# Optimization experiments

Hardware: AMD Instinct MI355X
Metric: run time of the kernel (lower is better)

The kernel has to match this reference:

```python
import jax, jax.numpy as jnp
import numpy as np

B, D, H, T = 8192, 256, 266, 20  # batch, dim, dim+10, num timesteps
LAMBDA = 1.0
SIGMA = 1.0
EPS = 1e-5  # torch BatchNorm1d default eps


def _bn(h, g, b):
    # training-mode BatchNorm1d: biased batch statistics over axis 0
    m = h.mean(0)
    v = h.var(0)
    return g * (h - m) * jax.lax.rsqrt(v + EPS) + b


def _hidden(x, W, b, g, be):
    return jax.nn.relu(_bn(x @ W.T + b, g, be))


def setup_inputs() -> dict:
    key = jax.random.key(0)
    ks = jax.random.split(key, 16)

    def n(k, shape, s=0.05):
        return jax.random.normal(k, shape, jnp.float32) * s

    inp = {}
    inp["x"] = jax.random.normal(ks[0], (B, D), jnp.float32)
    inp["xi"] = jax.random.normal(ks[1], (T, B, D), jnp.float32)
    inp["timegrid"] = jnp.linspace(0.0, 1.0, T + 1).astype(jnp.float32)
    # per-timestep stacks of Linear+BN params (i_h1, h1_h2, h2_o)
    inp["W1"] = n(ks[2], (T, H, D)); inp["b1"] = jnp.zeros((T, H), jnp.float32)
    inp["g1"] = jnp.ones((T, H), jnp.float32); inp["be1"] = jnp.zeros((T, H), jnp.float32)
    inp["W2"] = n(ks[3], (T, H, H)); inp["b2"] = jnp.zeros((T, H), jnp.float32)
    inp["g2"] = jnp.ones((T, H), jnp.float32); inp["be2"] = jnp.zeros((T, H), jnp.float32)
    inp["W3"] = n(ks[4], (T, D, H)); inp["b3"] = jnp.zeros((T, D), jnp.float32)
    # v0 network: hiddenLayer(D,H) -> hiddenLayer(H,H) -> hiddenLayer(H,1)
    inp["vW1"] = n(ks[5], (H, D)); inp["vb1"] = jnp.zeros((H,), jnp.float32)
    inp["vg1"] = jnp.ones((H,), jnp.float32); inp["vbe1"] = jnp.zeros((H,), jnp.float32)
    inp["vW2"] = n(ks[6], (H, H)); inp["vb2"] = jnp.zeros((H,), jnp.float32)
    inp["vg2"] = jnp.ones((H,), jnp.float32); inp["vbe2"] = jnp.zeros((H,), jnp.float32)
    inp["vW3"] = n(ks[7], (1, H)); inp["vb3"] = jnp.zeros((1,), jnp.float32)
    inp["vg3"] = jnp.ones((1,), jnp.float32); inp["vbe3"] = jnp.zeros((1,), jnp.float32)
    return inp


def reference(x, xi, timegrid, W1, b1, g1, be1, W2, b2, g2, be2, W3, b3,
              vW1, vb1, vg1, vbe1, vW2, vb2, vg2, vbe2, vW3, vb3, vg3, vbe3):
    # v0 sub-network evaluated on the initial x (i == 0 branch)
    v0 = _hidden(x, vW1, vb1, vg1, vbe1)
    v0 = _hidden(v0, vW2, vb2, vg2, vbe2)
    v0 = _hidden(v0, vW3, vb3, vg3, vbe3)  # [B, 1]

    hsteps = timegrid[1:] - timegrid[:-1]  # [T]

    def step(carry, inp_t):
        xt, vt = carry
        (W1t, b1t, g1t, be1t, W2t, b2t, g2t, be2t, W3t, b3t, ht, xit) = inp_t
        h1 = _hidden(xt, W1t, b1t, g1t, be1t)
        h2 = _hidden(h1, W2t, b2t, g2t, be2t)
        grad = h2 @ W3t.T + b3t                     # [B, D]
        alpha = -jnp.sqrt(LAMBDA) * grad
        f = jnp.sum(alpha * alpha, axis=1)          # ||alpha||_2^2 per row
        noise = SIGMA * jnp.sqrt(ht) * xit          # sigma*sqrt(h)*xi
        # diag(grad @ noise.T) == row-wise dot product (same math, O(B*D))
        dot = jnp.sum(grad * noise, axis=1)
        vt = vt - (f * ht)[:, None] + dot[:, None]
        xt = xt + alpha * ht + noise
        return (xt, vt), None

    (xT, vT), _ = jax.lax.scan(
        step, (x, v0),
        (W1, b1, g1, be1, W2, b2, g2, be2, W3, b3, hsteps, xi))
    return vT, xT
```

## Files before the change

kernel.cpp:

```cpp
#include <hip/hip_runtime.h>
#include <hip/hip_bf16.h>
#include <math.h>

#define BATCH 8192
#define DDIM 256
#define HDIM 266
#define NPAD 320
#define TSTEPS 20
#define BN_EPS 1e-5f
#define LAMBDA_C 1.0f
#define SIGMA_C 1.0f
#define LSTR 72

typedef __attribute__((ext_vector_type(8))) short short8;
typedef __attribute__((ext_vector_type(4))) float f32x4;

__device__ __forceinline__ short f2bf(float f) {
    __hip_bfloat16 h = __float2bfloat16(f);
    return *reinterpret_cast<short*>(&h);
}
__device__ __forceinline__ float bf2f(short s) {
    union { unsigned u; float f; } v;
    v.u = ((unsigned)(unsigned short)s) << 16;
    return v.f;
}

__global__ __launch_bounds__(256)
void pad_w_k(short* __restrict__ dst, const float* __restrict__ src,
             int total, int Npad, int N, int Kpad, int K)
{
    int idx = blockIdx.x * 256 + threadIdx.x;
    if (idx >= total) return;
    int k = idx % Kpad;
    int r = (idx / Kpad) % Npad;
    int t = idx / (Kpad * Npad);
    float v = (r < N && k < K) ? src[((size_t)t * N + r) * K + k] : 0.0f;
    dst[idx] = f2bf(v);
}

__global__ __launch_bounds__(256)
void pad_b_k(float* __restrict__ dst, const float* __restrict__ src,
             int total, int Npad, int N)
{
    int idx = blockIdx.x * 256 + threadIdx.x;
    if (idx >= total) return;
    int n = idx % Npad;
    int t = idx / Npad;
    dst[idx] = (n < N) ? src[(size_t)t * N + n] : 0.0f;
}

__global__ __launch_bounds__(256)
void init_k(const float* __restrict__ x, float* __restrict__ xt,
            short* __restrict__ xtb, float* __restrict__ zbase, int zcount)
{
    int i = blockIdx.x * 256 + threadIdx.x;
    if (i < BATCH * DDIM) { float v = x[i]; xt[i] = v; xtb[i] = f2bf(v); }
    if (i < zcount) zbase[i] = 0.0f;
}

__global__ __launch_bounds__(256)
void gemm_k(const short* __restrict__ A, int lda, int ktn,
            const short* __restrict__ W, int ldw,
            const float* __restrict__ biasp,
            short* __restrict__ C, int ldc,
            float* __restrict__ csum_out, float* __restrict__ csq_out, int nstats)
{
    __shared__ __align__(16) short As[64 * LSTR];
    __shared__ __align__(16) short Bs[64 * LSTR];

    const int tid  = threadIdx.x;
    const int col0 = blockIdx.x * 64;
    const int row0 = blockIdx.y * 64;
    const int lane = tid & 63;
    const int w    = tid >> 6;
    const int q    = lane >> 4;
    const int m    = lane & 15;
    const int wr   = (w >> 1) * 32;
    const int wc   = (w & 1) * 32;
    const int srow = tid >> 2;
    const int kq   = (tid & 3) * 8;

    f32x4 acc[2][2];
    #pragma unroll
    for (int i = 0; i < 2; ++i)
        #pragma unroll
        for (int j = 0; j < 2; ++j) acc[i][j] = (f32x4){0.f, 0.f, 0.f, 0.f};

    for (int kt = 0; kt < ktn; ++kt) {
        const int kg = kt * 64 + kq;
        const short* ap = A + (size_t)(row0 + srow) * lda + kg;
        const short* wp = W + (size_t)(col0 + srow) * ldw + kg;
        short8 a0 = *(const short8*)ap;
        short8 a1 = *(const short8*)(ap + 32);
        short8 w0 = *(const short8*)wp;
        short8 w1 = *(const short8*)(wp + 32);
        *(short8*)&As[srow * LSTR + kq]      = a0;
        *(short8*)&As[srow * LSTR + kq + 32] = a1;
        *(short8*)&Bs[srow * LSTR + kq]      = w0;
        *(short8*)&Bs[srow * LSTR + kq + 32] = w1;
        __syncthreads();

        #pragma unroll
        for (int kk = 0; kk < 2; ++kk) {
            short8 fa0 = *(const short8*)&As[(wr + m)      * LSTR + q * 8 + kk * 32];
            short8 fa1 = *(const short8*)&As[(wr + 16 + m) * LSTR + q * 8 + kk * 32];
            short8 fb0 = *(const short8*)&Bs[(wc + m)      * LSTR + q * 8 + kk * 32];
            short8 fb1 = *(const short8*)&Bs[(wc + 16 + m) * LSTR + q * 8 + kk * 32];
            acc[0][0] = __builtin_amdgcn_mfma_f32_16x16x32_bf16(fa0, fb0, acc[0][0], 0, 0, 0);
            acc[0][1] = __builtin_amdgcn_mfma_f32_16x16x32_bf16(fa0, fb1, acc[0][1], 0, 0, 0);
            acc[1][0] = __builtin_amdgcn_mfma_f32_16x16x32_bf16(fa1, fb0, acc[1][0], 0, 0, 0);
            acc[1][1] = __builtin_amdgcn_mfma_f32_16x16x32_bf16(fa1, fb1, acc[1][1], 0, 0, 0);
        }
        __syncthreads();
    }

    float cs[2], cq[2];
    #pragma unroll
    for (int j = 0; j < 2; ++j) {
        const int col = col0 + wc + j * 16 + m;
        const float bv = biasp[col];
        float s = 0.0f, sq = 0.0f;
        #pragma unroll
        for (int i = 0; i < 2; ++i)
            #pragma unroll
            for (int r = 0; r < 4; ++r) {
                float v = acc[i][j][r] + bv;
                int row = row0 + wr + i * 16 + q * 4 + r;
                C[(size_t)row * ldc + col] = f2bf(v);
                s += v; sq += v * v;
            }
        cs[j] = s; cq[j] = sq;
    }
    #pragma unroll
    for (int j = 0; j < 2; ++j) {
        cs[j] += __shfl_xor(cs[j], 16); cs[j] += __shfl_xor(cs[j], 32);
        cq[j] += __shfl_xor(cq[j], 16); cq[j] += __shfl_xor(cq[j], 32);
    }
    float* reds = (float*)As;
    float* redq = (float*)Bs;
    if (q == 0) {
        #pragma unroll
        for (int j = 0; j < 2; ++j) {
            reds[(w >> 1) * 64 + wc + j * 16 + m] = cs[j];
            redq[(w >> 1) * 64 + wc + j * 16 + m] = cq[j];
        }
    }
    __syncthreads();
    if (tid < 64) {
        int col = col0 + tid;
        if (col < nstats) {
            atomicAdd(&csum_out[col], reds[tid] + reds[64 + tid]);
            atomicAdd(&csq_out[col],  redq[tid] + redq[64 + tid]);
        }
    }
}

__global__ __launch_bounds__(256)
void bn_k(short* __restrict__ act,
          const float* __restrict__ csum, const float* __restrict__ csq,
          const float* __restrict__ g, const float* __restrict__ be)
{
    __shared__ float sS[NPAD];
    __shared__ float sT[NPAD];
    const int tid = threadIdx.x;
    for (int k = tid; k < NPAD; k += 256) {
        float s = 0.0f, t = 0.0f;
        if (k < HDIM) {
            float mn = csum[k] * (1.0f / BATCH);
            float vr = csq[k] * (1.0f / BATCH) - mn * mn;
            float rs = rsqrtf(fmaxf(vr, 0.0f) + BN_EPS);
            s = g[k] * rs;
            t = be[k] - mn * s;
        }
        sS[k] = s; sT[k] = t;
    }
    __syncthreads();
    const size_t base = (size_t)blockIdx.x * 32 * NPAD;
    #pragma unroll
    for (int c = 0; c < 5; ++c) {
        int flat = c * 256 + tid;
        int r  = flat / 40;
        int c8 = (flat % 40) * 8;
        short8 v = *(short8*)&act[base + (size_t)r * NPAD + c8];
        #pragma unroll
        for (int j = 0; j < 8; ++j) {
            float f = bf2f(v[j]);
            f = fmaxf(f * sS[c8 + j] + sT[c8 + j], 0.0f);
            v[j] = f2bf(f);
        }
        *(short8*)&act[base + (size_t)r * NPAD + c8] = v;
    }
}

__global__ __launch_bounds__(256)
void gemm_step3_k(const short* __restrict__ A,
                  const short* __restrict__ W,
                  const float* __restrict__ bias,
                  const float* __restrict__ xi_t,
                  float* __restrict__ xt,
                  short* __restrict__ xtb,
                  float* __restrict__ ftab, float* __restrict__ dtab,
                  const float* __restrict__ tg, int t)
{
    __shared__ __align__(16) short As[64 * LSTR];
    __shared__ __align__(16) short Bs[64 * LSTR];

    const int tid  = threadIdx.x;
    const int col0 = blockIdx.x * 64;
    const int row0 = blockIdx.y * 64;
    const int lane = tid & 63;
    const int w    = tid >> 6;
    const int q    = lane >> 4;
    const int m    = lane & 15;
    const int wr   = (w >> 1) * 32;
    const int wc   = (w & 1) * 32;
    const int srow = tid >> 2;
    const int kq   = (tid & 3) * 8;

    f32x4 acc[2][2];
    #pragma unroll
    for (int i = 0; i < 2; ++i)
        #pragma unroll
        for (int j = 0; j < 2; ++j) acc[i][j] = (f32x4){0.f, 0.f, 0.f, 0.f};

    for (int kt = 0; kt < 5; ++kt) {
        const int kg = kt * 64 + kq;
        const short* ap = A + (size_t)(row0 + srow) * NPAD + kg;
        const short* wp = W + (size_t)(col0 + srow) * NPAD + kg;
        short8 a0 = *(const short8*)ap;
        short8 a1 = *(const short8*)(ap + 32);
        short8 w0 = *(const short8*)wp;
        short8 w1 = *(const short8*)(wp + 32);
        *(short8*)&As[srow * LSTR + kq]      = a0;
        *(short8*)&As[srow * LSTR + kq + 32] = a1;
        *(short8*)&Bs[srow * LSTR + kq]      = w0;
        *(short8*)&Bs[srow * LSTR + kq + 32] = w1;
        __syncthreads();

        #pragma unroll
        for (int kk = 0; kk < 2; ++kk) {
            short8 fa0 = *(const short8*)&As[(wr + m)      * LSTR + q * 8 + kk * 32];
            short8 fa1 = *(const short8*)&As[(wr + 16 + m) * LSTR + q * 8 + kk * 32];
            short8 fb0 = *(const short8*)&Bs[(wc + m)      * LSTR + q * 8 + kk * 32];
            short8 fb1 = *(const short8*)&Bs[(wc + 16 + m) * LSTR + q * 8 + kk * 32];
            acc[0][0] = __builtin_amdgcn_mfma_f32_16x16x32_bf16(fa0, fb0, acc[0][0], 0, 0, 0);
            acc[0][1] = __builtin_amdgcn_mfma_f32_16x16x32_bf16(fa0, fb1, acc[0][1], 0, 0, 0);
            acc[1][0] = __builtin_amdgcn_mfma_f32_16x16x32_bf16(fa1, fb0, acc[1][0], 0, 0, 0);
            acc[1][1] = __builtin_amdgcn_mfma_f32_16x16x32_bf16(fa1, fb1, acc[1][1], 0, 0, 0);
        }
        __syncthreads();
    }

    const float ht  = tg[t + 1] - tg[t];
    const float sn  = SIGMA_C * sqrtf(ht);
    const float sql = sqrtf(LAMBDA_C);

    float fp[2][4], dp[2][4];
    #pragma unroll
    for (int i = 0; i < 2; ++i)
        #pragma unroll
        for (int r = 0; r < 4; ++r) {
            const int row = row0 + wr + i * 16 + q * 4 + r;
            float fr = 0.0f, dr = 0.0f;
            #pragma unroll
            for (int j = 0; j < 2; ++j) {
                const int col = col0 + wc + j * 16 + m;
                float grad = acc[i][j][r] + bias[col];
                size_t idx = (size_t)row * DDIM + col;
                float noise = sn * xi_t[idx];
                float nx = xt[idx] - sql * grad * ht + noise;
                xt[idx] = nx;
                xtb[idx] = f2bf(nx);
                fr += LAMBDA_C * grad * grad;
                dr += grad * noise;
            }
            fp[i][r] = fr; dp[i][r] = dr;
        }
    #pragma unroll
    for (int i = 0; i < 2; ++i)
        #pragma unroll
        for (int r = 0; r < 4; ++r) {
            fp[i][r] += __shfl_xor(fp[i][r], 1); dp[i][r] += __shfl_xor(dp[i][r], 1);
            fp[i][r] += __shfl_xor(fp[i][r], 2); dp[i][r] += __shfl_xor(dp[i][r], 2);
            fp[i][r] += __shfl_xor(fp[i][r], 4); dp[i][r] += __shfl_xor(dp[i][r], 4);
            fp[i][r] += __shfl_xor(fp[i][r], 8); dp[i][r] += __shfl_xor(dp[i][r], 8);
        }
    float* redf = (float*)As;
    float* redd = (float*)Bs;
    if (m == 0) {
        #pragma unroll
        for (int i = 0; i < 2; ++i)
            #pragma unroll
            for (int r = 0; r < 4; ++r) {
                redf[(w & 1) * 64 + wr + i * 16 + q * 4 + r] = fp[i][r];
                redd[(w & 1) * 64 + wr + i * 16 + q * 4 + r] = dp[i][r];
            }
    }
    __syncthreads();
    if (tid < 64) {
        atomicAdd(&ftab[row0 + tid], redf[tid] + redf[64 + tid]);
        atomicAdd(&dtab[row0 + tid], redd[tid] + redd[64 + tid]);
    }
}

__global__ __launch_bounds__(256)
void vrow_k(const short* __restrict__ a2v,
            const float* __restrict__ vW3p, const float* __restrict__ vb3,
            float* __restrict__ pre3, float* __restrict__ sum3, float* __restrict__ sumsq3)
{
    __shared__ float wred[8];
    const int tid = threadIdx.x;
    const int wave = tid >> 6, lane = tid & 63;
    const int row = blockIdx.x * 4 + wave;
    float sum = 0.0f;
    #pragma unroll
    for (int c = 0; c < 5; ++c) {
        int k = c * 64 + lane;
        sum += bf2f(a2v[(size_t)row * NPAD + k]) * vW3p[k];
    }
    sum += __shfl_xor(sum, 1);  sum += __shfl_xor(sum, 2);
    sum += __shfl_xor(sum, 4);  sum += __shfl_xor(sum, 8);
    sum += __shfl_xor(sum, 16); sum += __shfl_xor(sum, 32);
    if (lane == 0) {
        float p = sum + vb3[0];
        pre3[row] = p;
        wred[wave] = p;
        wred[4 + wave] = p * p;
    }
    __syncthreads();
    if (tid == 0) {
        atomicAdd(sum3,   wred[0] + wred[1] + wred[2] + wred[3]);
        atomicAdd(sumsq3, wred[4] + wred[5] + wred[6] + wred[7]);
    }
}

__global__ __launch_bounds__(256)
void v3b_k(const float* __restrict__ pre3,
           const float* __restrict__ sum3, const float* __restrict__ sumsq3,
           const float* __restrict__ vg3, const float* __restrict__ vbe3,
           float* __restrict__ vt)
{
    int i = blockIdx.x * 256 + threadIdx.x;
    float mn = sum3[0] * (1.0f / BATCH);
    float va = fmaxf(sumsq3[0] * (1.0f / BATCH) - mn * mn, 0.0f);
    float rs = rsqrtf(va + BN_EPS);
    if (i < BATCH) vt[i] = fmaxf(vg3[0] * (pre3[i] - mn) * rs + vbe3[0], 0.0f);
}

__global__ __launch_bounds__(256)
void final_v_k(const float* __restrict__ vt,
               const float* __restrict__ ftab, const float* __restrict__ dtab,
               const float* __restrict__ tg, float* __restrict__ outv)
{
    int i = blockIdx.x * 256 + threadIdx.x;
    if (i >= BATCH) return;
    float v = vt[i];
    for (int t = 0; t < TSTEPS; ++t) {
        float ht = tg[t + 1] - tg[t];
        v += dtab[(size_t)t * BATCH + i] - ftab[(size_t)t * BATCH + i] * ht;
    }
    outv[i] = v;
}

extern "C" void kernel_launch(void* const* d_in, const int* in_sizes, int n_in,
                              void* d_out, int out_size, void* d_ws, size_t ws_size,
                              hipStream_t stream)
{
    const float* x    = (const float*)d_in[0];
    const float* xi   = (const float*)d_in[1];
    const float* tg   = (const float*)d_in[2];
    const float* W1   = (const float*)d_in[3];
    const float* b1   = (const float*)d_in[4];
    const float* g1   = (const float*)d_in[5];
    const float* be1  = (const float*)d_in[6];
    const float* W2   = (const float*)d_in[7];
    const float* b2   = (const float*)d_in[8];
    const float* g2   = (const float*)d_in[9];
    const float* be2  = (const float*)d_in[10];
    const float* W3   = (const float*)d_in[11];
    const float* b3   = (const float*)d_in[12];
    const float* vW1  = (const float*)d_in[13];
    const float* vb1  = (const float*)d_in[14];
    const float* vg1  = (const float*)d_in[15];
    const float* vbe1 = (const float*)d_in[16];
    const float* vW2  = (const float*)d_in[17];
    const float* vb2  = (const float*)d_in[18];
    const float* vg2  = (const float*)d_in[19];
    const float* vbe2 = (const float*)d_in[20];
    const float* vW3  = (const float*)d_in[21];
    const float* vb3  = (const float*)d_in[22];
    const float* vg3  = (const float*)d_in[23];
    const float* vbe3 = (const float*)d_in[24];

    float* out = (float*)d_out;
    float* xt  = out + BATCH;

    short* xtb  = (short*)d_ws;
    short* hp1  = xtb + (size_t)BATCH * DDIM;
    short* hp2  = hp1 + (size_t)BATCH * NPAD;
    short* W1b  = hp2 + (size_t)BATCH * NPAD;
    short* W2b  = W1b + (size_t)TSTEPS * NPAD * DDIM;
    short* W3b  = W2b + (size_t)TSTEPS * NPAD * NPAD;
    short* vW1b = W3b + (size_t)TSTEPS * DDIM * NPAD;
    short* vW2b = vW1b + (size_t)NPAD * DDIM;
    float* fbase = (float*)(vW2b + (size_t)NPAD * NPAD);
    float* b1p  = fbase;
    float* b2p  = b1p + TSTEPS * NPAD;
    float* vb1p = b2p + TSTEPS * NPAD;
    float* vb2p = vb1p + NPAD;
    float* vW3p = vb2p + NPAD;
    float* vt   = vW3p + NPAD;
    float* pre3 = vt + BATCH;
    float* ftab = pre3 + BATCH;
    float* dtab = ftab + (size_t)TSTEPS * BATCH;
    float* csA  = dtab + (size_t)TSTEPS * BATCH;
    float* cqA  = csA + 21 * NPAD;
    float* csB  = cqA + 21 * NPAD;
    float* cqB  = csB + 21 * NPAD;
    float* s3   = cqB + 21 * NPAD;
    float* q3   = s3 + 1;
    const int zcount = 2 * TSTEPS * BATCH + 4 * 21 * NPAD + 2;

    dim3 blk(256);
    dim3 gH(5, BATCH / 64);
    dim3 gD(4, BATCH / 64);

    init_k<<<dim3((BATCH * DDIM + 255) / 256), blk, 0, stream>>>(x, xt, xtb, ftab, zcount);
    {
        int tot;
        tot = TSTEPS * NPAD * DDIM;
        pad_w_k<<<dim3((tot + 255) / 256), blk, 0, stream>>>(W1b, W1, tot, NPAD, HDIM, DDIM, DDIM);
        tot = TSTEPS * NPAD * NPAD;
        pad_w_k<<<dim3((tot + 255) / 256), blk, 0, stream>>>(W2b, W2, tot, NPAD, HDIM, NPAD, HDIM);
        tot = TSTEPS * DDIM * NPAD;
        pad_w_k<<<dim3((tot + 255) / 256), blk, 0, stream>>>(W3b, W3, tot, DDIM, DDIM, NPAD, HDIM);
        tot = NPAD * DDIM;
        pad_w_k<<<dim3((tot + 255) / 256), blk, 0, stream>>>(vW1b, vW1, tot, NPAD, HDIM, DDIM, DDIM);
        tot = NPAD * NPAD;
        pad_w_k<<<dim3((tot + 255) / 256), blk, 0, stream>>>(vW2b, vW2, tot, NPAD, HDIM, NPAD, HDIM);
        tot = TSTEPS * NPAD;
        pad_b_k<<<dim3((tot + 255) / 256), blk, 0, stream>>>(b1p, b1, tot, NPAD, HDIM);
        pad_b_k<<<dim3((tot + 255) / 256), blk, 0, stream>>>(b2p, b2, tot, NPAD, HDIM);
        pad_b_k<<<dim3(2), blk, 0, stream>>>(vb1p, vb1, NPAD, NPAD, HDIM);
        pad_b_k<<<dim3(2), blk, 0, stream>>>(vb2p, vb2, NPAD, NPAD, HDIM);
        pad_b_k<<<dim3(2), blk, 0, stream>>>(vW3p, vW3, NPAD, NPAD, HDIM);
    }

    float* csV1 = csA + 20 * NPAD; float* cqV1 = cqA + 20 * NPAD;
    float* csV2 = csB + 20 * NPAD; float* cqV2 = cqB + 20 * NPAD;
    gemm_k<<<gH, blk, 0, stream>>>(xtb, DDIM, 4, vW1b, DDIM, vb1p, hp1, NPAD, csV1, cqV1, HDIM);
    bn_k<<<dim3(256), blk, 0, stream>>>(hp1, csV1, cqV1, vg1, vbe1);
    gemm_k<<<gH, blk, 0, stream>>>(hp1, NPAD, 5, vW2b, NPAD, vb2p, hp2, NPAD, csV2, cqV2, HDIM);
    bn_k<<<dim3(256), blk, 0, stream>>>(hp2, csV2, cqV2, vg2, vbe2);
    vrow_k<<<dim3(BATCH / 4), blk, 0, stream>>>(hp2, vW3p, vb3, pre3, s3, q3);
    v3b_k<<<dim3(BATCH / 256), blk, 0, stream>>>(pre3, s3, q3, vg3, vbe3, vt);

    for (int t = 0; t < TSTEPS; ++t) {
        gemm_k<<<gH, blk, 0, stream>>>(
            xtb, DDIM, 4, W1b + (size_t)t * NPAD * DDIM, DDIM, b1p + t * NPAD,
            hp1, NPAD, csA + t * NPAD, cqA + t * NPAD, HDIM);
        bn_k<<<dim3(256), blk, 0, stream>>>(hp1, csA + t * NPAD, cqA + t * NPAD,
                                            g1 + t * HDIM, be1 + t * HDIM);
        gemm_k<<<gH, blk, 0, stream>>>(
            hp1, NPAD, 5, W2b + (size_t)t * NPAD * NPAD, NPAD, b2p + t * NPAD,
            hp2, NPAD, csB + t * NPAD, cqB + t * NPAD, HDIM);
        bn_k<<<dim3(256), blk, 0, stream>>>(hp2, csB + t * NPAD, cqB + t * NPAD,
                                            g2 + t * HDIM, be2 + t * HDIM);
        gemm_step3_k<<<gD, blk, 0, stream>>>(
            hp2, W3b + (size_t)t * DDIM * NPAD, b3 + t * DDIM,
            xi + (size_t)t * BATCH * DDIM, xt, xtb,
            ftab + (size_t)t * BATCH, dtab + (size_t)t * BATCH, tg, t);
    }
    final_v_k<<<dim3(BATCH / 256), blk, 0, stream>>>(vt, ftab, dtab, tg, out);
}
```

Measured before the change: 1.175 ms.

## Fuse BatchNorm+ReLU into consumer GEMM A-loads and register-prefetch tiles

Removes the standalone bn_k passes by applying BatchNorm scale/shift and ReLU while loading the A operand into shared memory in gemm2/gemm3 and vrow_k. The GEMMs gain register prefetch of the next K tile and new tile shapes (32x160, 32x128). The fp32 xt state is dropped in favour of the bf16 copy, with fp32 output written only on the last step. All pad kernels are merged into one prep launch. This saves two full read-modify-write passes over the hidden activations per step, plus launch overhead. The cost is more work in each GEMM and a possible precision change from carrying the state in bf16.

```diff
diff --git a/kernel.cpp b/kernel.cpp
--- a/kernel.cpp
+++ b/kernel.cpp
@@ -8,8 +8,6 @@
 #define NPAD 320
 #define TSTEPS 20
 #define BN_EPS 1e-5f
-#define LAMBDA_C 1.0f
-#define SIGMA_C 1.0f
 #define LSTR 72
 
 typedef __attribute__((ext_vector_type(8))) short short8;
@@ -25,60 +23,99 @@
     return v.f;
 }
 
-__global__ __launch_bounds__(256)
-void pad_w_k(short* __restrict__ dst, const float* __restrict__ src,
-             int total, int Npad, int N, int Kpad, int K)
-{
-    int idx = blockIdx.x * 256 + threadIdx.x;
-    if (idx >= total) return;
-    int k = idx % Kpad;
-    int r = (idx / Kpad) % Npad;
-    int t = idx / (Kpad * Npad);
-    float v = (r < N && k < K) ? src[((size_t)t * N + r) * K + k] : 0.0f;
-    dst[idx] = f2bf(v);
-}
-
-__global__ __launch_bounds__(256)
-void pad_b_k(float* __restrict__ dst, const float* __restrict__ src,
-             int total, int Npad, int N)
-{
-    int idx = blockIdx.x * 256 + threadIdx.x;
-    if (idx >= total) return;
-    int n = idx % Npad;
-    int t = idx / Npad;
-    dst[idx] = (n < N) ? src[(size_t)t * N + n] : 0.0f;
-}
-
-__global__ __launch_bounds__(256)
-void init_k(const float* __restrict__ x, float* __restrict__ xt,
-            short* __restrict__ xtb, float* __restrict__ zbase, int zcount)
+#define SZ_W1B (20L * 320 * 256)
+#define SZ_W2B (20L * 320 * 320)
+#define SZ_W3B (20L * 256 * 320)
+#define SZ_VW1 (320L * 256)
+#define SZ_VW2 (320L * 320)
+#define SZ_B1P (20L * 320)
+#define SZ_B2P (20L * 320)
+#define PREP_TOTAL (SZ_W1B + SZ_W2B + SZ_W3B + SZ_VW1 + SZ_VW2 + SZ_B1P + SZ_B2P + 3 * 320)
+
+__global__ __launch_bounds__(256)
+void prep_k(short* __restrict__ W1b, const float* __restrict__ W1,
+            short* __restrict__ W2b, const float* __restrict__ W2,
+            short* __restrict__ W3b, const float* __restrict__ W3,
+            short* __restrict__ vW1b, const float* __restrict__ vW1,
+            short* __restrict__ vW2b, const float* __restrict__ vW2,
+            float* __restrict__ b1p, const float* __restrict__ b1,
+            float* __restrict__ b2p, const float* __restrict__ b2,
+            float* __restrict__ vb1p, const float* __restrict__ vb1,
+            float* __restrict__ vb2p, const float* __restrict__ vb2,
+            float* __restrict__ vW3p, const float* __restrict__ vW3)
+{
+    long idx = (long)blockIdx.x * 256 + threadIdx.x;
+    if (idx < SZ_W1B) {
+        long k = idx % 256, r = (idx / 256) % 320, t = idx / (256L * 320);
+        float v = (r < HDIM) ? W1[((size_t)t * HDIM + r) * 256 + k] : 0.0f;
+        W1b[idx] = f2bf(v); return;
+    }
+    idx -= SZ_W1B;
+    if (idx < SZ_W2B) {
+        long k = idx % 320, r = (idx / 320) % 320, t = idx / (320L * 320);
+        float v = (r < HDIM && k < HDIM) ? W2[((size_t)t * HDIM + r) * HDIM + k] : 0.0f;
+        W2b[idx] = f2bf(v); return;
+    }
+    idx -= SZ_W2B;
+    if (idx < SZ_W3B) {
+        long k = idx % 320, r = (idx / 320) % 256, t = idx / (320L * 256);
+        float v = (k < HDIM) ? W3[((size_t)t * 256 + r) * HDIM + k] : 0.0f;
+        W3b[idx] = f2bf(v); return;
+    }
+    idx -= SZ_W3B;
+    if (idx < SZ_VW1) {
+        long k = idx % 256, r = idx / 256;
+        float v = (r < HDIM) ? vW1[(size_t)r * 256 + k] : 0.0f;
+        vW1b[idx] = f2bf(v); return;
+    }
+    idx -= SZ_VW1;
+    if (idx < SZ_VW2) {
+        long k = idx % 320, r = idx / 320;
+        float v = (r < HDIM && k < HDIM) ? vW2[(size_t)r * HDIM + k] : 0.0f;
+        vW2b[idx] = f2bf(v); return;
+    }
+    idx -= SZ_VW2;
+    if (idx < SZ_B1P) { long n = idx % 320, t = idx / 320;
+        b1p[idx] = (n < HDIM) ? b1[(size_t)t * HDIM + n] : 0.0f; return; }
+    idx -= SZ_B1P;
+    if (idx < SZ_B2P) { long n = idx % 320, t = idx / 320;
+        b2p[idx] = (n < HDIM) ? b2[(size_t)t * HDIM + n] : 0.0f; return; }
+    idx -= SZ_B2P;
+    if (idx < 320) { vb1p[idx] = (idx < HDIM) ? vb1[idx] : 0.0f; return; }
+    idx -= 320;
+    if (idx < 320) { vb2p[idx] = (idx < HDIM) ? vb2[idx] : 0.0f; return; }
+    idx -= 320;
+    if (idx < 320) { vW3p[idx] = (idx < HDIM) ? vW3[idx] : 0.0f; return; }
+}
+
+__global__ __launch_bounds__(256)
+void init_k(const float* __restrict__ x, short* __restrict__ xtb,
+            float* __restrict__ zbase, int zcount)
 {
     int i = blockIdx.x * 256 + threadIdx.x;
-    if (i < BATCH * DDIM) { float v = x[i]; xt[i] = v; xtb[i] = f2bf(v); }
+    if (i < BATCH * DDIM) xtb[i] = f2bf(x[i]);
     if (i < zcount) zbase[i] = 0.0f;
 }
 
 __global__ __launch_bounds__(256)
-void gemm_k(const short* __restrict__ A, int lda, int ktn,
-            const short* __restrict__ W, int ldw,
-            const float* __restrict__ biasp,
-            short* __restrict__ C, int ldc,
-            float* __restrict__ csum_out, float* __restrict__ csq_out, int nstats)
+void gemm1_k(const short* __restrict__ A, const short* __restrict__ W,
+             const float* __restrict__ biasp, short* __restrict__ C,
+             float* __restrict__ csum, float* __restrict__ csq)
 {
     __shared__ __align__(16) short As[64 * LSTR];
     __shared__ __align__(16) short Bs[64 * LSTR];
-
-    const int tid  = threadIdx.x;
-    const int col0 = blockIdx.x * 64;
-    const int row0 = blockIdx.y * 64;
-    const int lane = tid & 63;
-    const int w    = tid >> 6;
-    const int q    = lane >> 4;
-    const int m    = lane & 15;
-    const int wr   = (w >> 1) * 32;
-    const int wc   = (w & 1) * 32;
-    const int srow = tid >> 2;
-    const int kq   = (tid & 3) * 8;
+    const int tid = threadIdx.x;
+    const int col0 = blockIdx.x * 64, row0 = blockIdx.y * 64;
+    const int lane = tid & 63, w = tid >> 6, q = lane >> 4, m = lane & 15;
+    const int wr = (w >> 1) * 32, wc = (w & 1) * 32;
+    const int srow = tid >> 2, kq = (tid & 3) * 8;
+
+    const short* ap = A + (size_t)(row0 + srow) * DDIM + kq;
+    const short* wp = W + (size_t)(col0 + srow) * DDIM + kq;
+    short8 ra0 = *(const short8*)ap;
+    short8 ra1 = *(const short8*)(ap + 32);
+    short8 rw0 = *(const short8*)wp;
+    short8 rw1 = *(const short8*)(wp + 32);
 
     f32x4 acc[2][2];
     #pragma unroll
@@ -86,26 +123,24 @@
         #pragma unroll
         for (int j = 0; j < 2; ++j) acc[i][j] = (f32x4){0.f, 0.f, 0.f, 0.f};
 
-    for (int kt = 0; kt < ktn; ++kt) {
-        const int kg = kt * 64 + kq;
-        const short* ap = A + (size_t)(row0 + srow) * lda + kg;
-        const short* wp = W + (size_t)(col0 + srow) * ldw + kg;
-        short8 a0 = *(const short8*)ap;
-        short8 a1 = *(const short8*)(ap + 32);
-        short8 w0 = *(const short8*)wp;
-        short8 w1 = *(const short8*)(wp + 32);
-        *(short8*)&As[srow * LSTR + kq]      = a0;
-        *(short8*)&As[srow * LSTR + kq + 32] = a1;
-        *(short8*)&Bs[srow * LSTR + kq]      = w0;
-        *(short8*)&Bs[srow * LSTR + kq + 32] = w1;
+    #pragma unroll
+    for (int kt = 0; kt < 4; ++kt) {
+        *(short8*)&As[srow * LSTR + kq]      = ra0;
+        *(short8*)&As[srow * LSTR + kq + 32] = ra1;
+        *(short8*)&Bs[srow * LSTR + kq]      = rw0;
+        *(short8*)&Bs[srow * LSTR + kq + 32] = rw1;
         __syncthreads();
-
+        if (kt < 3) {
+            ap += 64; wp += 64;
+            ra0 = *(const short8*)ap; ra1 = *(const short8*)(ap + 32);
+            rw0 = *(const short8*)wp; rw1 = *(const short8*)(wp + 32);
+        }
         #pragma unroll
         for (int kk = 0; kk < 2; ++kk) {
-            short8 fa0 = *(const short8*)&As[(wr + m)      * LSTR + q * 8 + kk * 32];
-            short8 fa1 = *(const short8*)&As[(wr + 16 + m) * LSTR + q * 8 + kk * 32];
-            short8 fb0 = *(const short8*)&Bs[(wc + m)      * LSTR + q * 8 + kk * 32];
-            short8 fb1 = *(const short8*)&Bs[(wc + 16 + m) * LSTR + q * 8 + kk * 32];
+            short8 fa0 = *(const short8*)&As[(wr + m)      * LSTR + kk * 32 + q * 8];
+            short8 fa1 = *(const short8*)&As[(wr + 16 + m) * LSTR + kk * 32 + q * 8];
+            short8 fb0 = *(const short8*)&Bs[(wc + m)      * LSTR + kk * 32 + q * 8];
+            short8 fb1 = *(const short8*)&Bs[(wc + 16 + m) * LSTR + kk * 32 + q * 8];
             acc[0][0] = __builtin_amdgcn_mfma_f32_16x16x32_bf16(fa0, fb0, acc[0][0], 0, 0, 0);
             acc[0][1] = __builtin_amdgcn_mfma_f32_16x16x32_bf16(fa0, fb1, acc[0][1], 0, 0, 0);
             acc[1][0] = __builtin_amdgcn_mfma_f32_16x16x32_bf16(fa1, fb0, acc[1][0], 0, 0, 0);
@@ -126,7 +161,7 @@
             for (int r = 0; r < 4; ++r) {
                 float v = acc[i][j][r] + bv;
                 int row = row0 + wr + i * 16 + q * 4 + r;
-                C[(size_t)row * ldc + col] = f2bf(v);
+                C[(size_t)row * NPAD + col] = f2bf(v);
                 s += v; sq += v * v;
             }
         cs[j] = s; cq[j] = sq;
@@ -148,26 +183,30 @@
     __syncthreads();
     if (tid < 64) {
         int col = col0 + tid;
-        if (col < nstats) {
-            atomicAdd(&csum_out[col], reds[tid] + reds[64 + tid]);
-            atomicAdd(&csq_out[col],  redq[tid] + redq[64 + tid]);
-        }
-    }
-}
-
-__global__ __launch_bounds__(256)
-void bn_k(short* __restrict__ act,
-          const float* __restrict__ csum, const float* __restrict__ csq,
-          const float* __restrict__ g, const float* __restrict__ be)
-{
-    __shared__ float sS[NPAD];
-    __shared__ float sT[NPAD];
+        if (col < HDIM) {
+            atomicAdd(&csum[col], reds[tid] + reds[64 + tid]);
+            atomicAdd(&csq[col],  redq[tid] + redq[64 + tid]);
+        }
+    }
+}
+
+__global__ __launch_bounds__(256)
+void gemm2_k(const short* __restrict__ A, const short* __restrict__ W,
+             const float* __restrict__ biasp,
+             const float* __restrict__ csum_in, const float* __restrict__ csq_in,
+             const float* __restrict__ g, const float* __restrict__ be,
+             short* __restrict__ C,
+             float* __restrict__ csum_out, float* __restrict__ csq_out)
+{
+    __shared__ __align__(16) short As[32 * LSTR];
+    __shared__ __align__(16) short Bs[160 * LSTR];
+    __shared__ float sS[NPAD], sT[NPAD];
     const int tid = threadIdx.x;
     for (int k = tid; k < NPAD; k += 256) {
         float s = 0.0f, t = 0.0f;
         if (k < HDIM) {
-            float mn = csum[k] * (1.0f / BATCH);
-            float vr = csq[k] * (1.0f / BATCH) - mn * mn;
+            float mn = csum_in[k] * (1.0f / BATCH);
+            float vr = csq_in[k] * (1.0f / BATCH) - mn * mn;
             float rs = rsqrtf(fmaxf(vr, 0.0f) + BN_EPS);
             s = g[k] * rs;
             t = be[k] - mn * s;
@@ -175,148 +214,255 @@
         sS[k] = s; sT[k] = t;
     }
     __syncthreads();
-    const size_t base = (size_t)blockIdx.x * 32 * NPAD;
-    #pragma unroll
-    for (int c = 0; c < 5; ++c) {
-        int flat = c * 256 + tid;
-        int r  = flat / 40;
-        int c8 = (flat % 40) * 8;
-        short8 v = *(short8*)&act[base + (size_t)r * NPAD + c8];
+
+    const int col0 = blockIdx.x * 160, row0 = blockIdx.y * 32;
+    const int lane = tid & 63, w = tid >> 6, q = lane >> 4, m = lane & 15;
+    const int rh = w >> 1, ch = w & 1;
+    const int srowA = tid >> 3, kqA = (tid & 7) * 8;
+
+    const short* ap = A + (size_t)(row0 + srowA) * NPAD + kqA;
+    short8 rA = *(const short8*)ap;
+    short8 rB[5];
+    #pragma unroll
+    for (int i = 0; i < 5; ++i) {
+        int s = tid + 256 * i;
+        rB[i] = *(const short8*)(W + (size_t)(col0 + (s >> 3)) * NPAD + ((s & 7) * 8));
+    }
+
+    f32x4 acc[5];
+    #pragma unroll
+    for (int j = 0; j < 5; ++j) acc[j] = (f32x4){0.f, 0.f, 0.f, 0.f};
+
+    #pragma unroll
+    for (int kt = 0; kt < 5; ++kt) {
+        short8 ta;
+        const int kb = kt * 64 + kqA;
         #pragma unroll
         for (int j = 0; j < 8; ++j) {
-            float f = bf2f(v[j]);
-            f = fmaxf(f * sS[c8 + j] + sT[c8 + j], 0.0f);
-            v[j] = f2bf(f);
-        }
-        *(short8*)&act[base + (size_t)r * NPAD + c8] = v;
-    }
-}
-
-__global__ __launch_bounds__(256)
-void gemm_step3_k(const short* __restrict__ A,
-                  const short* __restrict__ W,
-                  const float* __restrict__ bias,
-                  const float* __restrict__ xi_t,
-                  float* __restrict__ xt,
-                  short* __restrict__ xtb,
-                  float* __restrict__ ftab, float* __restrict__ dtab,
-                  const float* __restrict__ tg, int t)
-{
-    __shared__ __align__(16) short As[64 * LSTR];
-    __shared__ __align__(16) short Bs[64 * LSTR];
-
-    const int tid  = threadIdx.x;
-    const int col0 = blockIdx.x * 64;
-    const int row0 = blockIdx.y * 64;
-    const int lane = tid & 63;
-    const int w    = tid >> 6;
-    const int q    = lane >> 4;
-    const int m    = lane & 15;
-    const int wr   = (w >> 1) * 32;
-    const int wc   = (w & 1) * 32;
-    const int srow = tid >> 2;
-    const int kq   = (tid & 3) * 8;
-
-    f32x4 acc[2][2];
-    #pragma unroll
-    for (int i = 0; i < 2; ++i)
-        #pragma unroll
-        for (int j = 0; j < 2; ++j) acc[i][j] = (f32x4){0.f, 0.f, 0.f, 0.f};
-
+            float f = bf2f(rA[j]);
+            f = fmaxf(f * sS[kb + j] + sT[kb + j], 0.0f);
+            ta[j] = f2bf(f);
+        }
+        *(short8*)&As[srowA * LSTR + kqA] = ta;
+        #pragma unroll
+        for (int i = 0; i < 5; ++i) {
+            int s = tid + 256 * i;
+            *(short8*)&Bs[(s >> 3) * LSTR + (s & 7) * 8] = rB[i];
+        }
+        __syncthreads();
+        if (kt < 4) {
+            ap += 64;
+            rA = *(const short8*)ap;
+            #pragma unroll
+            for (int i = 0; i < 5; ++i) {
+                int s = tid + 256 * i;
+                rB[i] = *(const short8*)(W + (size_t)(col0 + (s >> 3)) * NPAD
+                                         + (kt + 1) * 64 + ((s & 7) * 8));
+            }
+        }
+        #pragma unroll
+        for (int kk = 0; kk < 2; ++kk) {
+            short8 fa = *(const short8*)&As[(rh * 16 + m) * LSTR + kk * 32 + q * 8];
+            #pragma unroll
+            for (int j = 0; j < 5; ++j) {
+                short8 fb = *(const short8*)&Bs[(ch * 80 + j * 16 + m) * LSTR + kk * 32 + q * 8];
+                acc[j] = __builtin_amdgcn_mfma_f32_16x16x32_bf16(fa, fb, acc[j], 0, 0, 0);
+            }
+        }
+        __syncthreads();
+    }
+
+    float csv[5], cqv[5];
+    #pragma unroll
+    for (int j = 0; j < 5; ++j) {
+        const int col = col0 + ch * 80 + j * 16 + m;
+        const float bv = biasp[col];
+        float s = 0.0f, sq = 0.0f;
+        #pragma unroll
+        for (int r = 0; r < 4; ++r) {
+            float v = acc[j][r] + bv;
+            int row = row0 + rh * 16 + q * 4 + r;
+            C[(size_t)row * NPAD + col] = f2bf(v);
+            s += v; sq += v * v;
+        }
+        csv[j] = s; cqv[j] = sq;
+    }
+    #pragma unroll
+    for (int j = 0; j < 5; ++j) {
+        csv[j] += __shfl_xor(csv[j], 16); csv[j] += __shfl_xor(csv[j], 32);
+        cqv[j] += __shfl_xor(cqv[j], 16); cqv[j] += __shfl_xor(cqv[j], 32);
+    }
+    float* redS = (float*)As;
+    float* redQ = redS + 320;
+    if (q == 0) {
+        #pragma unroll
+        for (int j = 0; j < 5; ++j) {
+            redS[rh * 160 + ch * 80 + j * 16 + m] = csv[j];
+            redQ[rh * 160 + ch * 80 + j * 16 + m] = cqv[j];
+        }
+    }
+    __syncthreads();
+    if (tid < 160) {
+        int col = col0 + tid;
+        if (col < HDIM) {
+            atomicAdd(&csum_out[col], redS[tid] + redS[160 + tid]);
+            atomicAdd(&csq_out[col],  redQ[tid] + redQ[160 + tid]);
+        }
+    }
+}
+
+__global__ __launch_bounds__(256)
+void gemm3_k(const short* __restrict__ A, const short* __restrict__ W,
+             const float* __restrict__ bias,
+             const float* __restrict__ csum_in, const float* __restrict__ csq_in,
+             const float* __restrict__ g, const float* __restrict__ be,
+             const float* __restrict__ xi_t,
+             short* __restrict__ xtb, float* __restrict__ xout,
+             float* __restrict__ ftab, float* __restrict__ dtab,
+             const float* __restrict__ tg, int t, int last)
+{
+    __shared__ __align__(16) short As[32 * LSTR];
+    __shared__ __align__(16) short Bs[128 * LSTR];
+    __shared__ float sS[NPAD], sT[NPAD];
+    const int tid = threadIdx.x;
+    for (int k = tid; k < NPAD; k += 256) {
+        float s = 0.0f, tt = 0.0f;
+        if (k < HDIM) {
+            float mn = csum_in[k] * (1.0f / BATCH);
+            float vr = csq_in[k] * (1.0f / BATCH) - mn * mn;
+            float rs = rsqrtf(fmaxf(vr, 0.0f) + BN_EPS);
+            s = g[k] * rs;
+            tt = be[k] - mn * s;
+        }
+        sS[k] = s; sT[k] = tt;
+    }
+    __syncthreads();
+
+    const int col0 = blockIdx.x * 128, row0 = blockIdx.y * 32;
+    const int lane = tid & 63, w = tid >> 6, q = lane >> 4, m = lane & 15;
+    const int rh = w >> 1, ch = w & 1;
+    const int srowA = tid >> 3, kqA = (tid & 7) * 8;
+
+    const short* ap = A + (size_t)(row0 + srowA) * NPAD + kqA;
+    short8 rA = *(const short8*)ap;
+    short8 rB[4];
+    #pragma unroll
+    for (int i = 0; i < 4; ++i) {
+        int s = tid + 256 * i;
+        rB[i] = *(const short8*)(W + (size_t)(col0 + (s >> 3)) * NPAD + ((s & 7) * 8));
+    }
+
+    f32x4 acc[4];
+    #pragma unroll
+    for (int j = 0; j < 4; ++j) acc[j] = (f32x4){0.f, 0.f, 0.f, 0.f};
+
+    #pragma unroll
     for (int kt = 0; kt < 5; ++kt) {
-        const int kg = kt * 64 + kq;
-        const short* ap = A + (size_t)(row0 + srow) * NPAD + kg;
-        const short* wp = W + (size_t)(col0 + srow) * NPAD + kg;
-        short8 a0 = *(const short8*)ap;
-        short8 a1 = *(const short8*)(ap + 32);
-        short8 w0 = *(const short8*)wp;
-        short8 w1 = *(const short8*)(wp + 32);
-        *(short8*)&As[srow * LSTR + kq]      = a0;
-        *(short8*)&As[srow * LSTR + kq + 32] = a1;
-        *(short8*)&Bs[srow * LSTR + kq]      = w0;
-        *(short8*)&Bs[srow * LSTR + kq + 32] = w1;
+        short8 ta;
+        const int kb = kt * 64 + kqA;
+        #pragma unroll
+        for (int j = 0; j < 8; ++j) {
+            float f = bf2f(rA[j]);
+            f = fmaxf(f * sS[kb + j] + sT[kb + j], 0.0f);
+            ta[j] = f2bf(f);
+        }
+        *(short8*)&As[srowA * LSTR + kqA] = ta;
+        #pragma unroll
+        for (int i = 0; i < 4; ++i) {
+            int s = tid + 256 * i;
+            *(short8*)&Bs[(s >> 3) * LSTR + (s & 7) * 8] = rB[i];
+        }
         __syncthreads();
-
+        if (kt < 4) {
+            ap += 64;
+            rA = *(const short8*)ap;
+            #pragma unroll
+            for (int i = 0; i < 4; ++i) {
+                int s = tid + 256 * i;
+                rB[i] = *(const short8*)(W + (size_t)(col0 + (s >> 3)) * NPAD
+                                         + (kt + 1) * 64 + ((s & 7) * 8));
+            }
+        }
         #pragma unroll
         for (int kk = 0; kk < 2; ++kk) {
-            short8 fa0 = *(const short8*)&As[(wr + m)      * LSTR + q * 8 + kk * 32];
-            short8 fa1 = *(const short8*)&As[(wr + 16 + m) * LSTR + q * 8 + kk * 32];
-            short8 fb0 = *(const short8*)&Bs[(wc + m)      * LSTR + q * 8 + kk * 32];
-            short8 fb1 = *(const short8*)&Bs[(wc + 16 + m) * LSTR + q * 8 + kk * 32];
-            acc[0][0] = __builtin_amdgcn_mfma_f32_16x16x32_bf16(fa0, fb0, acc[0][0], 0, 0, 0);
-            acc[0][1] = __builtin_amdgcn_mfma_f32_16x16x32_bf16(fa0, fb1, acc[0][1], 0, 0, 0);
-            acc[1][0] = __builtin_amdgcn_mfma_f32_16x16x32_bf16(fa1, fb0, acc[1][0], 0, 0, 0);
-            acc[1][1] = __builtin_amdgcn_mfma_f32_16x16x32_bf16(fa1, fb1, acc[1][1], 0, 0, 0);
+            short8 fa = *(const short8*)&As[(rh * 16 + m) * LSTR + kk * 32 + q * 8];
+            #pragma unroll
+            for (int j = 0; j < 4; ++j) {
+                short8 fb = *(const short8*)&Bs[(ch * 64 + j * 16 + m) * LSTR + kk * 32 + q * 8];
+                acc[j] = __builtin_amdgcn_mfma_f32_16x16x32_bf16(fa, fb, acc[j], 0, 0, 0);
+            }
         }
         __syncthreads();
     }
 
-    const float ht  = tg[t + 1] - tg[t];
-    const float sn  = SIGMA_C * sqrtf(ht);
-    const float sql = sqrtf(LAMBDA_C);
-
-    float fp[2][4], dp[2][4];
-    #pragma unroll
-    for (int i = 0; i < 2; ++i)
+    const float ht = tg[t + 1] - tg[t];
+    const float sn = sqrtf(ht);
+    float fr[4] = {0.f, 0.f, 0.f, 0.f};
+    float dr[4] = {0.f, 0.f, 0.f, 0.f};
+    #pragma unroll
+    for (int j = 0; j < 4; ++j) {
+        const int col = col0 + ch * 64 + j * 16 + m;
+        const float bv = bias[col];
         #pragma unroll
         for (int r = 0; r < 4; ++r) {
-            const int row = row0 + wr + i * 16 + q * 4 + r;
-            float fr = 0.0f, dr = 0.0f;
-            #pragma unroll
-            for (int j = 0; j < 2; ++j) {
-                const int col = col0 + wc + j * 16 + m;
-                float grad = acc[i][j][r] + bias[col];
-                size_t idx = (size_t)row * DDIM + col;
-                float noise = sn * xi_t[idx];
-                float nx = xt[idx] - sql * grad * ht + noise;
-                xt[idx] = nx;
-                xtb[idx] = f2bf(nx);
-                fr += LAMBDA_C * grad * grad;
-                dr += grad * noise;
-            }
-            fp[i][r] = fr; dp[i][r] = dr;
-        }
-    #pragma unroll
-    for (int i = 0; i < 2; ++i)
+            const int row = row0 + rh * 16 + q * 4 + r;
+            size_t idx = (size_t)row * DDIM + col;
+            float grad = acc[j][r] + bv;
+            float noise = sn * xi_t[idx];
+            float nx = bf2f(xtb[idx]) - grad * ht + noise;
+            xtb[idx] = f2bf(nx);
+            if (last) xout[idx] = nx;
+            fr[r] += grad * grad;
+            dr[r] += grad * noise;
+        }
+    }
+    #pragma unroll
+    for (int r = 0; r < 4; ++r) {
+        fr[r] += __shfl_xor(fr[r], 1); dr[r] += __shfl_xor(dr[r], 1);
+        fr[r] += __shfl_xor(fr[r], 2); dr[r] += __shfl_xor(dr[r], 2);
+        fr[r] += __shfl_xor(fr[r], 4); dr[r] += __shfl_xor(dr[r], 4);
+        fr[r] += __shfl_xor(fr[r], 8); dr[r] += __shfl_xor(dr[r], 8);
+    }
+    if (m == 0) {
         #pragma unroll
         for (int r = 0; r < 4; ++r) {
-            fp[i][r] += __shfl_xor(fp[i][r], 1); dp[i][r] += __shfl_xor(dp[i][r], 1);
-            fp[i][r] += __shfl_xor(fp[i][r], 2); dp[i][r] += __shfl_xor(dp[i][r], 2);
-            fp[i][r] += __shfl_xor(fp[i][r], 4); dp[i][r] += __shfl_xor(dp[i][r], 4);
-            fp[i][r] += __shfl_xor(fp[i][r], 8); dp[i][r] += __shfl_xor(dp[i][r], 8);
-        }
-    float* redf = (float*)As;
-    float* redd = (float*)Bs;
-    if (m == 0) {
-        #pragma unroll
-        for (int i = 0; i < 2; ++i)
-            #pragma unroll
-            for (int r = 0; r < 4; ++r) {
-                redf[(w & 1) * 64 + wr + i * 16 + q * 4 + r] = fp[i][r];
-                redd[(w & 1) * 64 + wr + i * 16 + q * 4 + r] = dp[i][r];
-            }
-    }
-    __syncthreads();
-    if (tid < 64) {
-        atomicAdd(&ftab[row0 + tid], redf[tid] + redf[64 + tid]);
-        atomicAdd(&dtab[row0 + tid], redd[tid] + redd[64 + tid]);
-    }
-}
-
-__global__ __launch_bounds__(256)
-void vrow_k(const short* __restrict__ a2v,
+            const int row = row0 + rh * 16 + q * 4 + r;
+            atomicAdd(&ftab[row], fr[r]);
+            atomicAdd(&dtab[row], dr[r]);
+        }
+    }
+}
+
+__global__ __launch_bounds__(256)
+void vrow_k(const short* __restrict__ A,
+            const float* __restrict__ csum_in, const float* __restrict__ csq_in,
+            const float* __restrict__ g, const float* __restrict__ be,
             const float* __restrict__ vW3p, const float* __restrict__ vb3,
-            float* __restrict__ pre3, float* __restrict__ sum3, float* __restrict__ sumsq3)
-{
+            float* __restrict__ pre3, float* __restrict__ s3, float* __restrict__ q3)
+{
+    __shared__ float sS[NPAD], sT[NPAD];
     __shared__ float wred[8];
     const int tid = threadIdx.x;
+    for (int k = tid; k < NPAD; k += 256) {
+        float s = 0.0f, t = 0.0f;
+        if (k < HDIM) {
+            float mn = csum_in[k] * (1.0f / BATCH);
+            float vr = csq_in[k] * (1.0f / BATCH) - mn * mn;
+            float rs = rsqrtf(fmaxf(vr, 0.0f) + BN_EPS);
+            s = g[k] * rs;
+            t = be[k] - mn * s;
+        }
+        sS[k] = s; sT[k] = t;
+    }
+    __syncthreads();
     const int wave = tid >> 6, lane = tid & 63;
     const int row = blockIdx.x * 4 + wave;
     float sum = 0.0f;
     #pragma unroll
     for (int c = 0; c < 5; ++c) {
         int k = c * 64 + lane;
-        sum += bf2f(a2v[(size_t)row * NPAD + k]) * vW3p[k];
+        float v = fmaxf(bf2f(A[(size_t)row * NPAD + k]) * sS[k] + sT[k], 0.0f);
+        sum += v * vW3p[k];
     }
     sum += __shfl_xor(sum, 1);  sum += __shfl_xor(sum, 2);
     sum += __shfl_xor(sum, 4);  sum += __shfl_xor(sum, 8);
@@ -329,20 +475,20 @@
     }
     __syncthreads();
     if (tid == 0) {
-        atomicAdd(sum3,   wred[0] + wred[1] + wred[2] + wred[3]);
-        atomicAdd(sumsq3, wred[4] + wred[5] + wred[6] + wred[7]);
+        atomicAdd(s3, wred[0] + wred[1] + wred[2] + wred[3]);
+        atomicAdd(q3, wred[4] + wred[5] + wred[6] + wred[7]);
     }
 }
 
 __global__ __launch_bounds__(256)
 void v3b_k(const float* __restrict__ pre3,
-           const float* __restrict__ sum3, const float* __restrict__ sumsq3,
+           const float* __restrict__ s3, const float* __restrict__ q3,
            const float* __restrict__ vg3, const float* __restrict__ vbe3,
            float* __restrict__ vt)
 {
     int i = blockIdx.x * 256 + threadIdx.x;
-    float mn = sum3[0] * (1.0f / BATCH);
-    float va = fmaxf(sumsq3[0] * (1.0f / BATCH) - mn * mn, 0.0f);
+    float mn = s3[0] * (1.0f / BATCH);
+    float va = fmaxf(q3[0] * (1.0f / BATCH) - mn * mn, 0.0f);
     float rs = rsqrtf(va + BN_EPS);
     if (i < BATCH) vt[i] = fmaxf(vg3[0] * (pre3[i] - mn) * rs + vbe3[0], 0.0f);
 }
@@ -392,18 +538,18 @@
     const float* vg3  = (const float*)d_in[23];
     const float* vbe3 = (const float*)d_in[24];
 
-    float* out = (float*)d_out;
-    float* xt  = out + BATCH;
+    float* out  = (float*)d_out;
+    float* xout = out + BATCH;
 
     short* xtb  = (short*)d_ws;
     short* hp1  = xtb + (size_t)BATCH * DDIM;
     short* hp2  = hp1 + (size_t)BATCH * NPAD;
     short* W1b  = hp2 + (size_t)BATCH * NPAD;
-    short* W2b  = W1b + (size_t)TSTEPS * NPAD * DDIM;
-    short* W3b  = W2b + (size_t)TSTEPS * NPAD * NPAD;
-    short* vW1b = W3b + (size_t)TSTEPS * DDIM * NPAD;
-    short* vW2b = vW1b + (size_t)NPAD * DDIM;
-    float* fbase = (float*)(vW2b + (size_t)NPAD * NPAD);
+    short* W2b  = W1b + SZ_W1B;
+    short* W3b  = W2b + SZ_W2B;
+    short* vW1b = W3b + SZ_W3B;
+    short* vW2b = vW1b + SZ_VW1;
+    float* fbase = (float*)(vW2b + SZ_VW2);
     float* b1p  = fbase;
     float* b2p  = b1p + TSTEPS * NPAD;
     float* vb1p = b2p + TSTEPS * NPAD;
@@ -422,54 +568,38 @@
     const int zcount = 2 * TSTEPS * BATCH + 4 * 21 * NPAD + 2;
 
     dim3 blk(256);
-    dim3 gH(5, BATCH / 64);
-    dim3 gD(4, BATCH / 64);
-
-    init_k<<<dim3((BATCH * DDIM + 255) / 256), blk, 0, stream>>>(x, xt, xtb, ftab, zcount);
-    {
-        int tot;
-        tot = TSTEPS * NPAD * DDIM;
-        pad_w_k<<<dim3((tot + 255) / 256), blk, 0, stream>>>(W1b, W1, tot, NPAD, HDIM, DDIM, DDIM);
-        tot = TSTEPS * NPAD * NPAD;
-        pad_w_k<<<dim3((tot + 255) / 256), blk, 0, stream>>>(W2b, W2, tot, NPAD, HDIM, NPAD, HDIM);
-        tot = TSTEPS * DDIM * NPAD;
-        pad_w_k<<<dim3((tot + 255) / 256), blk, 0, stream>>>(W3b, W3, tot, DDIM, DDIM, NPAD, HDIM);
-        tot = NPAD * DDIM;
-        pad_w_k<<<dim3((tot + 255) / 256), blk, 0, stream>>>(vW1b, vW1, tot, NPAD, HDIM, DDIM, DDIM);
-        tot = NPAD * NPAD;
-        pad_w_k<<<dim3((tot + 255) / 256), blk, 0, stream>>>(vW2b, vW2, tot, NPAD, HDIM, NPAD, HDIM);
-        tot = TSTEPS * NPAD;
-        pad_b_k<<<dim3((tot + 255) / 256), blk, 0, stream>>>(b1p, b1, tot, NPAD, HDIM);
-        pad_b_k<<<dim3((tot + 255) / 256), blk, 0, stream>>>(b2p, b2, tot, NPAD, HDIM);
-        pad_b_k<<<dim3(2), blk, 0, stream>>>(vb1p, vb1, NPAD, NPAD, HDIM);
-        pad_b_k<<<dim3(2), blk, 0, stream>>>(vb2p, vb2, NPAD, NPAD, HDIM);
-        pad_b_k<<<dim3(2), blk, 0, stream>>>(vW3p, vW3, NPAD, NPAD, HDIM);
-    }
+    dim3 g1g(5, BATCH / 64);
+    dim3 g2g(2, BATCH / 32);
+    dim3 g3g(2, BATCH / 32);
+
+    init_k<<<dim3((BATCH * DDIM + 255) / 256), blk, 0, stream>>>(x, xtb, ftab, zcount);
+    prep_k<<<dim3((int)((PREP_TOTAL + 255) / 256)), blk, 0, stream>>>(
+        W1b, W1, W2b, W2, W3b, W3, vW1b, vW1, vW2b, vW2,
+        b1p, b1, b2p, b2, vb1p, vb1, vb2p, vb2, vW3p, vW3);
 
     float* csV1 = csA + 20 * NPAD; float* cqV1 = cqA + 20 * NPAD;
     float* csV2 = csB + 20 * NPAD; float* cqV2 = cqB + 20 * NPAD;
-    gemm_k<<<gH, blk, 0, stream>>>(xtb, DDIM, 4, vW1b, DDIM, vb1p, hp1, NPAD, csV1, cqV1, HDIM);
-    bn_k<<<dim3(256), blk, 0, stream>>>(hp1, csV1, cqV1, vg1, vbe1);
-    gemm_k<<<gH, blk, 0, stream>>>(hp1, NPAD, 5, vW2b, NPAD, vb2p, hp2, NPAD, csV2, cqV2, HDIM);
-    bn_k<<<dim3(256), blk, 0, stream>>>(hp2, csV2, cqV2, vg2, vbe2);
-    vrow_k<<<dim3(BATCH / 4), blk, 0, stream>>>(hp2, vW3p, vb3, pre3, s3, q3);
+    gemm1_k<<<g1g, blk, 0, stream>>>(xtb, vW1b, vb1p, hp1, csV1, cqV1);
+    gemm2_k<<<g2g, blk, 0, stream>>>(hp1, vW2b, vb2p, csV1, cqV1, vg1, vbe1,
+                                     hp2, csV2, cqV2);
+    vrow_k<<<dim3(BATCH / 4), blk, 0, stream>>>(hp2, csV2, cqV2, vg2, vbe2,
+                                                vW3p, vb3, pre3, s3, q3);
     v3b_k<<<dim3(BATCH / 256), blk, 0, stream>>>(pre3, s3, q3, vg3, vbe3, vt);
 
     for (int t = 0; t < TSTEPS; ++t) {
-        gemm_k<<<gH, blk, 0, stream>>>(
-            xtb, DDIM, 4, W1b + (size_t)t * NPAD * DDIM, DDIM, b1p + t * NPAD,
-            hp1, NPAD, csA + t * NPAD, cqA + t * NPAD, HDIM);
-        bn_k<<<dim3(256), blk, 0, stream>>>(hp1, csA + t * NPAD, cqA + t * NPAD,
-                                            g1 + t * HDIM, be1 + t * HDIM);
-        gemm_k<<<gH, blk, 0, stream>>>(
-            hp1, NPAD, 5, W2b + (size_t)t * NPAD * NPAD, NPAD, b2p + t * NPAD,
-            hp2, NPAD, csB + t * NPAD, cqB + t * NPAD, HDIM);
-        bn_k<<<dim3(256), blk, 0, stream>>>(hp2, csB + t * NPAD, cqB + t * NPAD,
-                                            g2 + t * HDIM, be2 + t * HDIM);
-        gemm_step3_k<<<gD, blk, 0, stream>>>(
+        gemm1_k<<<g1g, blk, 0, stream>>>(
+            xtb, W1b + (size_t)t * NPAD * DDIM, b1p + t * NPAD,
+            hp1, csA + t * NPAD, cqA + t * NPAD);
+        gemm2_k<<<g2g, blk, 0, stream>>>(
+            hp1, W2b + (size_t)t * NPAD * NPAD, b2p + t * NPAD,
+            csA + t * NPAD, cqA + t * NPAD, g1 + t * HDIM, be1 + t * HDIM,
+            hp2, csB + t * NPAD, cqB + t * NPAD);
+        gemm3_k<<<g3g, blk, 0, stream>>>(
             hp2, W3b + (size_t)t * DDIM * NPAD, b3 + t * DDIM,
-            xi + (size_t)t * BATCH * DDIM, xt, xtb,
-            ftab + (size_t)t * BATCH, dtab + (size_t)t * BATCH, tg, t);
+            csB + t * NPAD, cqB + t * NPAD, g2 + t * HDIM, be2 + t * HDIM,
+            xi + (size_t)t * BATCH * DDIM, xtb, xout,
+            ftab + (size_t)t * BATCH, dtab + (size_t)t * BATCH,
+            tg, t, (t == TSTEPS - 1) ? 1 : 0);
     }
     final_v_k<<<dim3(BATCH / 256), blk, 0, stream>>>(vt, ftab, dtab, tg, out);
 }
```

Result: faster. 1.144 ms (-2.7%).
